# Kernel optimization log

Hardware: AMD Instinct MI355X
Metric: run time of the kernel (lower is better)

The kernel has to match this reference:

```python
import jax, jax.numpy as jnp
import numpy as np
import math

B, N, D_IN, D_V, H, D_FF = 8, 2048, 256, 256, 8, 512
HD = D_V // H  # head dim = 32
EPS = 1e-5


def layernorm(x, g, b):
    mu = jnp.mean(x, axis=-1, keepdims=True)
    var = jnp.mean(jnp.square(x - mu), axis=-1, keepdims=True)
    return (x - mu) * jax.lax.rsqrt(var + EPS) * g + b


def setup_inputs() -> dict:
    key = jax.random.key(0)
    ks = jax.random.split(key, 12)
    s = 1.0 / math.sqrt(D_IN)
    return {
        "x": jax.random.normal(ks[0], (B, N, D_IN), jnp.float32),
        "y": jax.random.normal(ks[1], (B, N, D_IN), jnp.float32),
        "Wq": jax.random.normal(ks[2], (D_IN, D_V), jnp.float32) * s,
        "bq": jnp.zeros((D_V,), jnp.float32),
        "Wk": jax.random.normal(ks[3], (D_IN, D_V), jnp.float32) * s,
        "bk": jnp.zeros((D_V,), jnp.float32),
        "Wv": jax.random.normal(ks[4], (D_IN, D_V), jnp.float32) * s,
        "bv": jnp.zeros((D_V,), jnp.float32),
        "W1": jax.random.normal(ks[5], (D_V, D_FF), jnp.float32) * s,
        "b1": jnp.zeros((D_FF,), jnp.float32),
        "W2": jax.random.normal(ks[6], (D_FF, D_V), jnp.float32) * (1.0 / math.sqrt(D_FF)),
        "b2": jnp.zeros((D_V,), jnp.float32),
        "ln0_g": jnp.ones((D_IN,), jnp.float32),
        "ln0_b": jnp.zeros((D_IN,), jnp.float32),
        "ln1_g": jnp.ones((D_V,), jnp.float32),
        "ln1_b": jnp.zeros((D_V,), jnp.float32),
    }


def reference(x, y, Wq, bq, Wk, bk, Wv, bv, W1, b1, W2, b2, ln0_g, ln0_b, ln1_g, ln1_b):
    xn = layernorm(x, ln0_g, ln0_b)                      # ln0 on queries
    Q = (xn @ Wq + bq).reshape(B, N, H, HD)              # [B,Nq,H,hd]
    K = (y @ Wk + bk).reshape(B, N, H, HD)
    V = (y @ Wv + bv).reshape(B, N, H, HD)
    # NOTE: faithful scale = 1/sqrt(dim_V) (full model dim), not head dim
    S = jnp.einsum("bqhd,bkhd->bhqk", Q, K) / math.sqrt(D_V)
    A = jax.nn.softmax(S, axis=-1)
    O = Q + jnp.einsum("bhqk,bkhd->bqhd", A, V)          # per-head residual Q_ + A
    O = O.reshape(B, N, D_V)
    On = layernorm(O, ln1_g, ln1_b)
    ff = jax.nn.gelu(On @ W1 + b1, approximate=False) @ W2 + b2
    return O + ff
```

## Files before the change

### kernel.cpp

```cpp
#include <hip/hip_runtime.h>
#include <math.h>

#define RTOT 16384
#define NSEQ 2048
#define NHEAD 8
#define HDIM 32
#define QSCALE 0.09017132252479462f

typedef __attribute__((ext_vector_type(8))) short short8;
typedef __attribute__((ext_vector_type(4))) float f32x4;

#define GLOBAL_AS(p) ((__attribute__((address_space(1))) void*)(p))
#define LDS_AS(p) ((__attribute__((address_space(3))) void*)(p))

__device__ __forceinline__ unsigned pack_bf16(float a, float b) {
  unsigned ua = __float_as_uint(a) + 0x8000u;
  unsigned ub = __float_as_uint(b) + 0x8000u;
  return (ua >> 16) | (ub & 0xffff0000u);
}
__device__ __forceinline__ ushort bf16_1(float a) {
  return (ushort)((__float_as_uint(a) + 0x8000u) >> 16);
}

__global__ __launch_bounds__(256) void stage0_kernel(
    const float* __restrict__ x, const float* __restrict__ y,
    const float* __restrict__ Wq, const float* __restrict__ Wk,
    const float* __restrict__ Wv, const float* __restrict__ W1,
    const float* __restrict__ W2, const float* __restrict__ ln0g,
    const float* __restrict__ ln0b, ushort* __restrict__ Wqt,
    ushort* __restrict__ Wkt, ushort* __restrict__ Wvt,
    ushort* __restrict__ W1t, ushort* __restrict__ W2t,
    ushort* __restrict__ yh, ushort* __restrict__ xh) {
  const int bid = blockIdx.x;
  const int t = threadIdx.x;
  if (bid < 112) {
    const float* W;
    ushort* Wt;
    int K, N, tile;
    if (bid < 16) { W = Wq; Wt = Wqt; K = 256; N = 256; tile = bid; }
    else if (bid < 32) { W = Wk; Wt = Wkt; K = 256; N = 256; tile = bid - 16; }
    else if (bid < 48) { W = Wv; Wt = Wvt; K = 256; N = 256; tile = bid - 32; }
    else if (bid < 80) { W = W1; Wt = W1t; K = 256; N = 512; tile = bid - 48; }
    else { W = W2; Wt = W2t; K = 512; N = 256; tile = bid - 80; }
    const int tn = N >> 6;
    const int k0 = (tile / tn) << 6, n0 = (tile % tn) << 6;
    __shared__ float T[64][65];
#pragma unroll
    for (int i = 0; i < 16; ++i) {
      const int idx = t + i * 256;
      const int r = idx >> 6, c = idx & 63;
      T[r][c] = W[(size_t)(k0 + r) * N + n0 + c];
    }
    __syncthreads();
#pragma unroll
    for (int i = 0; i < 16; ++i) {
      const int idx = t + i * 256;
      const int r = idx >> 6, c = idx & 63;
      Wt[(size_t)(n0 + r) * K + k0 + c] = bf16_1(T[c][r]);
    }
  } else if (bid < 4208) {
    const size_t i = ((size_t)(bid - 112) * 256 + t) * 4;
    const float4 v = *(const float4*)&y[i];
    uint2 pk;
    pk.x = pack_bf16(v.x, v.y);
    pk.y = pack_bf16(v.z, v.w);
    *(uint2*)&yh[i] = pk;
  } else {
    const int lane = t & 63, wave = t >> 6;
    const size_t row = (size_t)(bid - 4208) * 4 + wave;
    const float* xr = x + row * 256;
    float4 v = *(const float4*)&xr[lane * 4];
    float s = v.x + v.y + v.z + v.w;
#pragma unroll
    for (int m = 1; m < 64; m <<= 1) s += __shfl_xor(s, m, 64);
    const float mu = s * (1.0f / 256.0f);
    const float dx = v.x - mu, dy = v.y - mu, dz = v.z - mu, dw = v.w - mu;
    float ss = dx * dx + dy * dy + dz * dz + dw * dw;
#pragma unroll
    for (int m = 1; m < 64; m <<= 1) ss += __shfl_xor(ss, m, 64);
    const float rstd = rsqrtf(ss * (1.0f / 256.0f) + 1e-5f);
    const float4 gv = *(const float4*)&ln0g[lane * 4];
    const float4 bv = *(const float4*)&ln0b[lane * 4];
    uint2 pk;
    pk.x = pack_bf16(dx * rstd * gv.x + bv.x, dy * rstd * gv.y + bv.y);
    pk.y = pack_bf16(dz * rstd * gv.z + bv.z, dw * rstd * gv.w + bv.w);
    *(uint2*)&xh[row * 256 + lane * 4] = pk;
  }
}

__global__ __launch_bounds__(256) void ln_kernel(
    const float* __restrict__ X, const float* __restrict__ g,
    const float* __restrict__ bt, ushort* __restrict__ Yh) {
  const int lane = threadIdx.x & 63;
  const int wave = threadIdx.x >> 6;
  const size_t row = (size_t)blockIdx.x * 4 + wave;
  const float* xr = X + row * 256;
  float4 v = *(const float4*)&xr[lane * 4];
  float s = v.x + v.y + v.z + v.w;
#pragma unroll
  for (int m = 1; m < 64; m <<= 1) s += __shfl_xor(s, m, 64);
  const float mu = s * (1.0f / 256.0f);
  const float dx = v.x - mu, dy = v.y - mu, dz = v.z - mu, dw = v.w - mu;
  float ss = dx * dx + dy * dy + dz * dz + dw * dw;
#pragma unroll
  for (int m = 1; m < 64; m <<= 1) ss += __shfl_xor(ss, m, 64);
  const float rstd = rsqrtf(ss * (1.0f / 256.0f) + 1e-5f);
  const float4 gv = *(const float4*)&g[lane * 4];
  const float4 bv = *(const float4*)&bt[lane * 4];
  uint2 pk;
  pk.x = pack_bf16(dx * rstd * gv.x + bv.x, dy * rstd * gv.y + bv.y);
  pk.y = pack_bf16(dz * rstd * gv.z + bv.z, dw * rstd * gv.w + bv.w);
  *(uint2*)&Yh[row * 256 + lane * 4] = pk;
}

template <int MODE>
__global__ __launch_bounds__(256) void mgemm_kernel(
    const ushort* __restrict__ A, const ushort* __restrict__ Wt,
    const ushort* __restrict__ Wt2, const float* __restrict__ bias,
    const float* __restrict__ bias2, const float* __restrict__ res,
    float* __restrict__ Cf, ushort* __restrict__ Ch, ushort* __restrict__ Ch2,
    float scale, int K, int N) {
  __shared__ ushort As[128 * 32];
  __shared__ ushort Bs[64 * 32];
  const int t = threadIdx.x;
  const int lane = t & 63, wave = t >> 6;
  const int l16 = lane & 15, quad = lane >> 4;
  const int row0 = blockIdx.x * 128;
  int ny = blockIdx.y;
  const ushort* W = Wt;
  const float* bs = bias;
  ushort* Co = Ch;
  if (MODE == 1 && ny >= (N >> 6)) {
    W = Wt2; bs = bias2; Co = Ch2; ny -= (N >> 6);
  }
  const int n0 = ny << 6;
  const int mrow = (wave & 1) * 64, ncol = (wave >> 1) * 32;

  const ushort* gA0 = A + (size_t)(row0 + (t >> 2)) * K + ((t & 3) << 3);
  const ushort* gA1 = gA0 + (size_t)64 * K;
  const ushort* gB = W + (size_t)(n0 + (t >> 2)) * K + ((t & 3) << 3);
  ushort* lA0 = As + 8 * t;
  ushort* lA1 = As + 2048 + 8 * t;
  ushort* lB = Bs + 8 * t;

  f32x4 acc[4][2] = {};
  for (int kc = 0; kc < K; kc += 32) {
    __builtin_amdgcn_global_load_lds(GLOBAL_AS(gA0 + kc), LDS_AS(lA0), 16, 0, 0);
    __builtin_amdgcn_global_load_lds(GLOBAL_AS(gA1 + kc), LDS_AS(lA1), 16, 0, 0);
    __builtin_amdgcn_global_load_lds(GLOBAL_AS(gB + kc), LDS_AS(lB), 16, 0, 0);
    __syncthreads();
    short8 af[4], bfr[2];
#pragma unroll
    for (int mi = 0; mi < 4; ++mi)
      af[mi] = *(const short8*)&As[(mrow + mi * 16 + l16) * 32 + quad * 8];
#pragma unroll
    for (int nj = 0; nj < 2; ++nj)
      bfr[nj] = *(const short8*)&Bs[(ncol + nj * 16 + l16) * 32 + quad * 8];
#pragma unroll
    for (int mi = 0; mi < 4; ++mi)
#pragma unroll
      for (int nj = 0; nj < 2; ++nj)
        acc[mi][nj] = __builtin_amdgcn_mfma_f32_16x16x32_bf16(
            af[mi], bfr[nj], acc[mi][nj], 0, 0, 0);
    __syncthreads();
  }
#pragma unroll
  for (int nj = 0; nj < 2; ++nj) {
    const int n = n0 + ncol + nj * 16 + l16;
    const float bv = bs[n];
#pragma unroll
    for (int mi = 0; mi < 4; ++mi) {
#pragma unroll
      for (int r = 0; r < 4; ++r) {
        const size_t m = (size_t)row0 + mrow + mi * 16 + quad * 4 + r;
        float v = acc[mi][nj][r] + bv;
        if (MODE == 2) v = 0.5f * v * (1.0f + erff(v * 0.70710678118654752f));
        if (MODE == 3) v += res[m * N + n];
        if (MODE == 0 || MODE == 3) Cf[m * N + n] = v;
        if (MODE == 0) Co[m * N + n] = bf16_1(v * scale);
        if (MODE == 1 || MODE == 2) Co[m * N + n] = bf16_1(v);
      }
    }
  }
}

__global__ __launch_bounds__(256) void attn_kernel(
    const float* __restrict__ Qf, const ushort* __restrict__ Qh,
    const ushort* __restrict__ Kh, const ushort* __restrict__ Vh,
    float* __restrict__ O) {
  __shared__ ushort Ks[2][64][40];
  __shared__ ushort Vt[2][32][72];
  __shared__ ushort Pl[4][16][72];

  const int t = threadIdx.x;
  const int lane = t & 63, wave = t >> 6;
  const int l16 = lane & 15, quad = lane >> 4;
  const int bh = blockIdx.x & 63;
  const int qt = blockIdx.x >> 6;
  const int b = bh >> 3, h = bh & 7;

  const size_t rowQ = (size_t)(b * NSEQ + qt * 64 + wave * 16 + l16);
  const short8 qfrag = *(const short8*)&Qh[rowQ * 256 + h * HDIM + quad * 8];
  const short8 ones = {16256, 16256, 16256, 16256,
                       16256, 16256, 16256, 16256};
  const f32x4 cinit = {-8.f, -8.f, -8.f, -8.f};

  f32x4 oacc0 = {0.f, 0.f, 0.f, 0.f}, oacc1 = {0.f, 0.f, 0.f, 0.f};
  f32x4 oaccS = {0.f, 0.f, 0.f, 0.f};

  const int kr = t >> 2, kc8 = (t & 3) << 3;
  const int vr = lane, vc8 = wave << 3;

  for (int kt = 0; kt < 32; ++kt) {
    const int bf = kt & 1;
    const size_t kbase = (size_t)(b * NSEQ + kt * 64);
    *(float4*)&Ks[bf][kr][kc8] =
        *(const float4*)&Kh[(kbase + kr) * 256 + h * HDIM + kc8];
    {
      const short8 vv = *(const short8*)&Vh[(kbase + vr) * 256 + h * HDIM + vc8];
#pragma unroll
      for (int i = 0; i < 8; ++i) Vt[bf][vc8 + i][vr] = (ushort)vv[i];
    }
    __syncthreads();

    f32x4 sa[4];
#pragma unroll
    for (int sub = 0; sub < 4; ++sub) {
      const short8 kf = *(const short8*)&Ks[bf][sub * 16 + l16][quad * 8];
      sa[sub] = __builtin_amdgcn_mfma_f32_16x16x32_bf16(kf, qfrag, cinit, 0, 0, 0);
    }
#pragma unroll
    for (int sub = 0; sub < 4; ++sub) {
      float p0 = __builtin_amdgcn_exp2f(sa[sub][0]);
      float p1 = __builtin_amdgcn_exp2f(sa[sub][1]);
      float p2 = __builtin_amdgcn_exp2f(sa[sub][2]);
      float p3 = __builtin_amdgcn_exp2f(sa[sub][3]);
      uint2 pk;
      pk.x = pack_bf16(p0, p1);
      pk.y = pack_bf16(p2, p3);
      *(uint2*)&Pl[wave][l16][sub * 16 + quad * 4] = pk;
    }
    __threadfence_block();

    const short8 pf0 = *(const short8*)&Pl[wave][l16][quad * 8];
    const short8 pf1 = *(const short8*)&Pl[wave][l16][32 + quad * 8];
    const short8 vf00 = *(const short8*)&Vt[bf][l16][quad * 8];
    const short8 vf01 = *(const short8*)&Vt[bf][l16][32 + quad * 8];
    const short8 vf10 = *(const short8*)&Vt[bf][16 + l16][quad * 8];
    const short8 vf11 = *(const short8*)&Vt[bf][16 + l16][32 + quad * 8];
    oacc0 = __builtin_amdgcn_mfma_f32_16x16x32_bf16(pf0, vf00, oacc0, 0, 0, 0);
    oacc0 = __builtin_amdgcn_mfma_f32_16x16x32_bf16(pf1, vf01, oacc0, 0, 0, 0);
    oacc1 = __builtin_amdgcn_mfma_f32_16x16x32_bf16(pf0, vf10, oacc1, 0, 0, 0);
    oacc1 = __builtin_amdgcn_mfma_f32_16x16x32_bf16(pf1, vf11, oacc1, 0, 0, 0);
    oaccS = __builtin_amdgcn_mfma_f32_16x16x32_bf16(pf0, ones, oaccS, 0, 0, 0);
    oaccS = __builtin_amdgcn_mfma_f32_16x16x32_bf16(pf1, ones, oaccS, 0, 0, 0);
  }

  const size_t row0 = (size_t)(b * NSEQ + qt * 64 + wave * 16 + quad * 4);
#pragma unroll
  for (int r = 0; r < 4; ++r) {
    const float il = 1.0f / oaccS[r];
    const size_t ro = (row0 + r) * 256 + h * HDIM + l16;
    O[ro] = Qf[ro] + oacc0[r] * il;
    O[ro + 16] = Qf[ro + 16] + oacc1[r] * il;
  }
}

extern "C" void kernel_launch(void* const* d_in, const int* in_sizes, int n_in,
                              void* d_out, int out_size, void* d_ws, size_t ws_size,
                              hipStream_t stream) {
  const float* x = (const float*)d_in[0];
  const float* y = (const float*)d_in[1];
  const float* Wq = (const float*)d_in[2];
  const float* bq = (const float*)d_in[3];
  const float* Wk = (const float*)d_in[4];
  const float* bk = (const float*)d_in[5];
  const float* Wv = (const float*)d_in[6];
  const float* bv = (const float*)d_in[7];
  const float* W1 = (const float*)d_in[8];
  const float* b1 = (const float*)d_in[9];
  const float* W2 = (const float*)d_in[10];
  const float* b2 = (const float*)d_in[11];
  const float* ln0g = (const float*)d_in[12];
  const float* ln0b = (const float*)d_in[13];
  const float* ln1g = (const float*)d_in[14];
  const float* ln1b = (const float*)d_in[15];
  float* out = (float*)d_out;
  char* base = (char*)d_ws;

  const size_t RM = (size_t)RTOT * 256;
  float* Ob = (float*)base;
  float* Qf = (float*)(base + RM * 4);
  ushort* yh = (ushort*)(base + RM * 4);
  ushort* Qh = (ushort*)(base + 2 * RM * 4);
  ushort* Kh = (ushort*)(base + 2 * RM * 4 + RM * 2);
  ushort* Vh = (ushort*)(base + 3 * RM * 4);
  ushort* xh = (ushort*)(base + 3 * RM * 4 + RM * 2);
  ushort* Onh = xh;
  ushort* Hidh = Qh;
  char* wbase = base + 4 * RM * 4;
  ushort* Wqt = (ushort*)wbase;
  ushort* Wkt = Wqt + 65536;
  ushort* Wvt = Wkt + 65536;
  ushort* W1t = Wvt + 65536;
  ushort* W2t = W1t + 131072;

  stage0_kernel<<<8304, 256, 0, stream>>>(x, y, Wq, Wk, Wv, W1, W2, ln0g, ln0b,
                                          Wqt, Wkt, Wvt, W1t, W2t, yh, xh);
  mgemm_kernel<1><<<dim3(128, 8), 256, 0, stream>>>(
      yh, Wkt, Wvt, bk, bv, nullptr, nullptr, Kh, Vh, 1.f, 256, 256);
  mgemm_kernel<0><<<dim3(128, 4), 256, 0, stream>>>(
      xh, Wqt, nullptr, bq, nullptr, nullptr, Qf, Qh, nullptr, QSCALE, 256, 256);
  attn_kernel<<<2048, 256, 0, stream>>>(Qf, Qh, Kh, Vh, Ob);
  ln_kernel<<<RTOT / 4, 256, 0, stream>>>(Ob, ln1g, ln1b, Onh);
  mgemm_kernel<2><<<dim3(128, 8), 256, 0, stream>>>(
      Onh, W1t, nullptr, b1, nullptr, nullptr, nullptr, Hidh, nullptr, 1.f, 256, 512);
  mgemm_kernel<3><<<dim3(128, 4), 256, 0, stream>>>(
      Hidh, W2t, nullptr, b2, nullptr, Ob, out, nullptr, nullptr, 1.f, 512, 256);
}
```

Measured before the change: 252.1 us.

## Fuse QKV projections into one launch and store V transposed for attention

Merges the K/V and Q projection GEMMs into a single qkv kernel with a 12-wide grid. The V projection now writes a per-head transposed layout through an LDS staging tile, so the attention kernel can load V tiles with vector stores instead of scattered per-element transposes. Attention also register-prefetches the next K/V tile during compute. Costs are the extra LDS transpose in the V epilogue, a workspace reshuffle (yh moved to the Ob region), and higher register pressure from the prefetch.

```diff
diff --git a/kernel.cpp b/kernel.cpp
--- a/kernel.cpp
+++ b/kernel.cpp
@@ -113,32 +113,119 @@
   *(uint2*)&Yh[row * 256 + lane * 4] = pk;
 }
 
+__global__ __launch_bounds__(256) void qkv_kernel(
+    const ushort* __restrict__ xh, const ushort* __restrict__ yh,
+    const ushort* __restrict__ Wqt, const ushort* __restrict__ Wkt,
+    const ushort* __restrict__ Wvt, const float* __restrict__ bq,
+    const float* __restrict__ bk, const float* __restrict__ bv,
+    float* __restrict__ Qf, ushort* __restrict__ Qh,
+    ushort* __restrict__ Kh, ushort* __restrict__ VhT) {
+  __shared__ union UU {
+    struct { ushort As[128 * 32]; ushort Bs[64 * 32]; } s;
+    ushort Ct[64 * 136];
+  } u;
+  const int t = threadIdx.x;
+  const int lane = t & 63, wave = t >> 6;
+  const int l16 = lane & 15, quad = lane >> 4;
+  const int row0 = blockIdx.x * 128;
+  const int ny = blockIdx.y;
+  const int which = ny >> 2;
+  const int n0 = (ny & 3) << 6;
+  const ushort* A = (which == 2) ? xh : yh;
+  const ushort* W = (which == 0) ? Wkt : (which == 1) ? Wvt : Wqt;
+  const float* bs = (which == 0) ? bk : (which == 1) ? bv : bq;
+  const int mrow = (wave & 1) * 64, ncol = (wave >> 1) * 32;
+
+  const ushort* gA0 = A + (size_t)(row0 + (t >> 2)) * 256 + ((t & 3) << 3);
+  const ushort* gA1 = gA0 + (size_t)64 * 256;
+  const ushort* gB = W + (size_t)(n0 + (t >> 2)) * 256 + ((t & 3) << 3);
+  ushort* lA0 = u.s.As + 8 * t;
+  ushort* lA1 = u.s.As + 2048 + 8 * t;
+  ushort* lB = u.s.Bs + 8 * t;
+
+  f32x4 acc[4][2] = {};
+  for (int kc = 0; kc < 256; kc += 32) {
+    __builtin_amdgcn_global_load_lds(GLOBAL_AS(gA0 + kc), LDS_AS(lA0), 16, 0, 0);
+    __builtin_amdgcn_global_load_lds(GLOBAL_AS(gA1 + kc), LDS_AS(lA1), 16, 0, 0);
+    __builtin_amdgcn_global_load_lds(GLOBAL_AS(gB + kc), LDS_AS(lB), 16, 0, 0);
+    __syncthreads();
+    short8 af[4], bfr[2];
+#pragma unroll
+    for (int mi = 0; mi < 4; ++mi)
+      af[mi] = *(const short8*)&u.s.As[(mrow + mi * 16 + l16) * 32 + quad * 8];
+#pragma unroll
+    for (int nj = 0; nj < 2; ++nj)
+      bfr[nj] = *(const short8*)&u.s.Bs[(ncol + nj * 16 + l16) * 32 + quad * 8];
+#pragma unroll
+    for (int mi = 0; mi < 4; ++mi)
+#pragma unroll
+      for (int nj = 0; nj < 2; ++nj)
+        acc[mi][nj] = __builtin_amdgcn_mfma_f32_16x16x32_bf16(
+            af[mi], bfr[nj], acc[mi][nj], 0, 0, 0);
+    __syncthreads();
+  }
+
+  if (which == 1) {
+#pragma unroll
+    for (int nj = 0; nj < 2; ++nj) {
+      const int nloc = ncol + nj * 16 + l16;
+      const float bvv = bs[n0 + nloc];
+#pragma unroll
+      for (int mi = 0; mi < 4; ++mi)
+#pragma unroll
+        for (int r = 0; r < 4; ++r)
+          u.Ct[nloc * 136 + mrow + mi * 16 + quad * 4 + r] =
+              bf16_1(acc[mi][nj][r] + bvv);
+    }
+    __syncthreads();
+    const int bb = row0 >> 11, ns0 = row0 & 2047;
+#pragma unroll
+    for (int i = 0; i < 4; ++i) {
+      const int c = t + i * 256;
+      const int rr = c >> 4, c8 = (c & 15) << 3;
+      *(float4*)&VhT[(size_t)(bb * 256 + n0 + rr) * 2048 + ns0 + c8] =
+          *(const float4*)&u.Ct[rr * 136 + c8];
+    }
+  } else {
+#pragma unroll
+    for (int nj = 0; nj < 2; ++nj) {
+      const int n = n0 + ncol + nj * 16 + l16;
+      const float bvv = bs[n];
+#pragma unroll
+      for (int mi = 0; mi < 4; ++mi) {
+#pragma unroll
+        for (int r = 0; r < 4; ++r) {
+          const size_t m = (size_t)row0 + mrow + mi * 16 + quad * 4 + r;
+          const float v = acc[mi][nj][r] + bvv;
+          if (which == 2) {
+            Qf[m * 256 + n] = v;
+            Qh[m * 256 + n] = bf16_1(v * QSCALE);
+          } else {
+            Kh[m * 256 + n] = bf16_1(v);
+          }
+        }
+      }
+    }
+  }
+}
+
 template <int MODE>
 __global__ __launch_bounds__(256) void mgemm_kernel(
     const ushort* __restrict__ A, const ushort* __restrict__ Wt,
-    const ushort* __restrict__ Wt2, const float* __restrict__ bias,
-    const float* __restrict__ bias2, const float* __restrict__ res,
-    float* __restrict__ Cf, ushort* __restrict__ Ch, ushort* __restrict__ Ch2,
-    float scale, int K, int N) {
+    const float* __restrict__ bias, const float* __restrict__ res,
+    float* __restrict__ Cf, ushort* __restrict__ Ch, int K, int N) {
   __shared__ ushort As[128 * 32];
   __shared__ ushort Bs[64 * 32];
   const int t = threadIdx.x;
   const int lane = t & 63, wave = t >> 6;
   const int l16 = lane & 15, quad = lane >> 4;
   const int row0 = blockIdx.x * 128;
-  int ny = blockIdx.y;
-  const ushort* W = Wt;
-  const float* bs = bias;
-  ushort* Co = Ch;
-  if (MODE == 1 && ny >= (N >> 6)) {
-    W = Wt2; bs = bias2; Co = Ch2; ny -= (N >> 6);
-  }
-  const int n0 = ny << 6;
+  const int n0 = blockIdx.y << 6;
   const int mrow = (wave & 1) * 64, ncol = (wave >> 1) * 32;
 
   const ushort* gA0 = A + (size_t)(row0 + (t >> 2)) * K + ((t & 3) << 3);
   const ushort* gA1 = gA0 + (size_t)64 * K;
-  const ushort* gB = W + (size_t)(n0 + (t >> 2)) * K + ((t & 3) << 3);
+  const ushort* gB = Wt + (size_t)(n0 + (t >> 2)) * K + ((t & 3) << 3);
   ushort* lA0 = As + 8 * t;
   ushort* lA1 = As + 2048 + 8 * t;
   ushort* lB = Bs + 8 * t;
@@ -167,18 +254,18 @@
 #pragma unroll
   for (int nj = 0; nj < 2; ++nj) {
     const int n = n0 + ncol + nj * 16 + l16;
-    const float bv = bs[n];
+    const float bvv = bias[n];
 #pragma unroll
     for (int mi = 0; mi < 4; ++mi) {
 #pragma unroll
       for (int r = 0; r < 4; ++r) {
         const size_t m = (size_t)row0 + mrow + mi * 16 + quad * 4 + r;
-        float v = acc[mi][nj][r] + bv;
-        if (MODE == 2) v = 0.5f * v * (1.0f + erff(v * 0.70710678118654752f));
-        if (MODE == 3) v += res[m * N + n];
-        if (MODE == 0 || MODE == 3) Cf[m * N + n] = v;
-        if (MODE == 0) Co[m * N + n] = bf16_1(v * scale);
-        if (MODE == 1 || MODE == 2) Co[m * N + n] = bf16_1(v);
+        float v = acc[mi][nj][r] + bvv;
+        if (MODE == 2) {
+          v = 0.5f * v * (1.0f + erff(v * 0.70710678118654752f));
+          Ch[m * N + n] = bf16_1(v);
+        }
+        if (MODE == 3) Cf[m * N + n] = v + res[m * N + n];
       }
     }
   }
@@ -186,7 +273,7 @@
 
 __global__ __launch_bounds__(256) void attn_kernel(
     const float* __restrict__ Qf, const ushort* __restrict__ Qh,
-    const ushort* __restrict__ Kh, const ushort* __restrict__ Vh,
+    const ushort* __restrict__ Kh, const ushort* __restrict__ VhT,
     float* __restrict__ O) {
   __shared__ ushort Ks[2][64][40];
   __shared__ ushort Vt[2][32][72];
@@ -209,19 +296,22 @@
   f32x4 oaccS = {0.f, 0.f, 0.f, 0.f};
 
   const int kr = t >> 2, kc8 = (t & 3) << 3;
-  const int vr = lane, vc8 = wave << 3;
+  const int vd = t >> 3, vc8 = (t & 7) << 3;
+  const ushort* gK = Kh + ((size_t)(b * NSEQ + kr)) * 256 + h * HDIM + kc8;
+  const ushort* gV = VhT + ((size_t)(bh * 32 + vd)) * 2048 + vc8;
+
+  float4 kreg = *(const float4*)gK;
+  float4 vreg = *(const float4*)gV;
 
   for (int kt = 0; kt < 32; ++kt) {
     const int bf = kt & 1;
-    const size_t kbase = (size_t)(b * NSEQ + kt * 64);
-    *(float4*)&Ks[bf][kr][kc8] =
-        *(const float4*)&Kh[(kbase + kr) * 256 + h * HDIM + kc8];
-    {
-      const short8 vv = *(const short8*)&Vh[(kbase + vr) * 256 + h * HDIM + vc8];
-#pragma unroll
-      for (int i = 0; i < 8; ++i) Vt[bf][vc8 + i][vr] = (ushort)vv[i];
-    }
-    __syncthreads();
+    *(float4*)&Ks[bf][kr][kc8] = kreg;
+    *(float4*)&Vt[bf][vd][vc8] = vreg;
+    __syncthreads();
+    if (kt < 31) {
+      kreg = *(const float4*)(gK + (size_t)(kt + 1) * 64 * 256);
+      vreg = *(const float4*)(gV + (kt + 1) * 64);
+    }
 
     f32x4 sa[4];
 #pragma unroll
@@ -289,12 +379,12 @@
   char* base = (char*)d_ws;
 
   const size_t RM = (size_t)RTOT * 256;
+  ushort* yh = (ushort*)base;
   float* Ob = (float*)base;
   float* Qf = (float*)(base + RM * 4);
-  ushort* yh = (ushort*)(base + RM * 4);
   ushort* Qh = (ushort*)(base + 2 * RM * 4);
   ushort* Kh = (ushort*)(base + 2 * RM * 4 + RM * 2);
-  ushort* Vh = (ushort*)(base + 3 * RM * 4);
+  ushort* VhT = (ushort*)(base + 3 * RM * 4);
   ushort* xh = (ushort*)(base + 3 * RM * 4 + RM * 2);
   ushort* Onh = xh;
   ushort* Hidh = Qh;
@@ -307,14 +397,12 @@
 
   stage0_kernel<<<8304, 256, 0, stream>>>(x, y, Wq, Wk, Wv, W1, W2, ln0g, ln0b,
                                           Wqt, Wkt, Wvt, W1t, W2t, yh, xh);
-  mgemm_kernel<1><<<dim3(128, 8), 256, 0, stream>>>(
-      yh, Wkt, Wvt, bk, bv, nullptr, nullptr, Kh, Vh, 1.f, 256, 256);
-  mgemm_kernel<0><<<dim3(128, 4), 256, 0, stream>>>(
-      xh, Wqt, nullptr, bq, nullptr, nullptr, Qf, Qh, nullptr, QSCALE, 256, 256);
-  attn_kernel<<<2048, 256, 0, stream>>>(Qf, Qh, Kh, Vh, Ob);
+  qkv_kernel<<<dim3(128, 12), 256, 0, stream>>>(xh, yh, Wqt, Wkt, Wvt, bq, bk,
+                                                bv, Qf, Qh, Kh, VhT);
+  attn_kernel<<<2048, 256, 0, stream>>>(Qf, Qh, Kh, VhT, Ob);
   ln_kernel<<<RTOT / 4, 256, 0, stream>>>(Ob, ln1g, ln1b, Onh);
-  mgemm_kernel<2><<<dim3(128, 8), 256, 0, stream>>>(
-      Onh, W1t, nullptr, b1, nullptr, nullptr, nullptr, Hidh, nullptr, 1.f, 256, 512);
-  mgemm_kernel<3><<<dim3(128, 4), 256, 0, stream>>>(
-      Hidh, W2t, nullptr, b2, nullptr, Ob, out, nullptr, nullptr, 1.f, 512, 256);
-}
+  mgemm_kernel<2><<<dim3(128, 8), 256, 0, stream>>>(Onh, W1t, b1, nullptr,
+                                                    nullptr, Hidh, 256, 512);
+  mgemm_kernel<3><<<dim3(128, 4), 256, 0, stream>>>(Hidh, W2t, b2, Ob, out,
+                                                    nullptr, 512, 256);
+}
```

New measurement: 235.0 us. -6.8%, faster.
